# Performance work log

Hardware: AMD Instinct MI355X
Metric: run time of the kernel (lower is better)

The kernel has to match this reference:

```python
import jax, jax.numpy as jnp
import numpy as np

D_MODEL = 1024
NHEADS = 16
DK = D_MODEL // NHEADS  # 64
B, LQ, LK = 4, 1024, 1024


def setup_inputs() -> dict:
    key = jax.random.key(0)
    ks = jax.random.split(key, 5)
    q = jax.random.normal(ks[0], (B, LQ, NHEADS, DK), dtype=jnp.float32)
    k = jax.random.normal(ks[1], (B, LK, NHEADS, DK), dtype=jnp.float32)
    v = jax.random.normal(ks[2], (B, LK, NHEADS, DK), dtype=jnp.float32)
    # LazyLinear materializes with in_features = LK * NHEADS due to the
    # source bug (it projects the reshaped raw score tensor, not attn@V).
    fc_w = jax.random.normal(ks[3], (D_MODEL, LK * NHEADS), dtype=jnp.float32) * 0.02
    fc_b = jax.random.normal(ks[4], (D_MODEL,), dtype=jnp.float32) * 0.02
    return {"q": q, "k": k, "v": v, "fc_w": fc_w, "fc_b": fc_b}


def reference(q, k, v, fc_w, fc_b):
    # Raw scaled scores: [b, i, j, n]
    scores = jnp.einsum('bink,bjnk->bijn', q, k) / np.float32(np.sqrt(DK))
    # NOTE (faithful to source): the softmax(dim=1) and the attn@V einsum are
    # computed in the original but their result is discarded; the output is
    # built from the raw scores. v does not influence the output.
    b, i = scores.shape[0], scores.shape[1]
    out = scores.reshape(b, i, -1)            # [b, i, j*n]
    out = out @ fc_w.T + fc_b                 # Linear(j*n -> d_model)
    return out
```

## Files before the change

### kernel.cpp

```cpp
#include <hip/hip_runtime.h>
#include <hip/hip_bf16.h>


typedef unsigned short u16;
typedef unsigned int u32;
typedef __bf16 bf16x8 __attribute__((ext_vector_type(8)));
typedef float f32x4 __attribute__((ext_vector_type(4)));

__device__ __forceinline__ u16 f2bf(float f) {
  union { float f; unsigned u; } in;
  in.f = f;
  unsigned u = in.u;
  u += 0x7fffu + ((u >> 16) & 1u);
  return (u16)(u >> 16);
}

__global__ __launch_bounds__(256) void prep_qk(const float* __restrict__ q,
                                               const float* __restrict__ k,
                                               u16* __restrict__ Qb,
                                               u16* __restrict__ Kt) {
  __shared__ u16 lds[64][65];
  const int tid = threadIdx.x;
  const int bid = blockIdx.x;

  if (bid < 1024) {
    int idx = bid * 256 + tid;
    float4 r[4];
#pragma unroll
    for (int it = 0; it < 4; ++it)
      r[it] = reinterpret_cast<const float4*>(q)[it * 262144 + idx];
#pragma unroll
    for (int it = 0; it < 4; ++it) {
      ushort4 o;
      o.x = f2bf(r[it].x); o.y = f2bf(r[it].y);
      o.z = f2bf(r[it].z); o.w = f2bf(r[it].w);
      reinterpret_cast<ushort4*>(Qb)[it * 262144 + idx] = o;
    }
  } else {
    int e = bid - 1024;
    int jt = e & 15, n = (e >> 4) & 15, b = e >> 8;
    const int j0 = jt * 64;
    float4 r[4];
#pragma unroll
    for (int it = 0; it < 4; ++it) {
      int idx = it * 256 + tid;
      int jj = idx >> 4;
      int c4 = idx & 15;
      r[it] = *reinterpret_cast<const float4*>(
          &k[(((size_t)b * 1024 + j0 + jj) * 16 + n) * 64 + c4 * 4]);
    }
#pragma unroll
    for (int it = 0; it < 4; ++it) {
      int idx = it * 256 + tid;
      int jj = idx >> 4;
      int c4 = idx & 15;
      lds[c4 * 4 + 0][jj] = f2bf(r[it].x);
      lds[c4 * 4 + 1][jj] = f2bf(r[it].y);
      lds[c4 * 4 + 2][jj] = f2bf(r[it].z);
      lds[c4 * 4 + 3][jj] = f2bf(r[it].w);
    }
    __syncthreads();
    ushort4 o[4];
#pragma unroll
    for (int it = 0; it < 4; ++it) {
      int idx = it * 256 + tid;
      int kk = idx >> 4;
      int c4 = idx & 15;
      o[it].x = lds[kk][c4 * 4 + 0]; o[it].y = lds[kk][c4 * 4 + 1];
      o[it].z = lds[kk][c4 * 4 + 2]; o[it].w = lds[kk][c4 * 4 + 3];
    }
#pragma unroll
    for (int it = 0; it < 4; ++it) {
      int idx = it * 256 + tid;
      int kk = idx >> 4;
      int c4 = idx & 15;
      *reinterpret_cast<ushort4*>(
          &Kt[((size_t)n * 256 + b * 64 + kk) * 1024 + j0 + c4 * 4]) = o[it];
    }
  }
}

__global__ __launch_bounds__(256) void prep_w(const float* __restrict__ w,
                                              u16* __restrict__ Wt) {
  __shared__ u16 lds[16 * 520];
  u32* lds32 = reinterpret_cast<u32*>(lds);
  const int tid = threadIdx.x;
  const int d = blockIdx.x >> 1;
  const int h = blockIdx.x & 1;
  const float* src = w + (size_t)d * 16384 + h * 8192;

  float4 ra[4], rb[4];
  const int gbase = ((tid >> 2) << 3) + (tid & 3);
#pragma unroll
  for (int it = 0; it < 4; ++it) {
    int g1 = it * 512 + gbase;
    ra[it] = reinterpret_cast<const float4*>(src)[g1];
    rb[it] = reinterpret_cast<const float4*>(src)[g1 + 4];
  }
  const int n0 = (tid & 3) * 4;
#pragma unroll
  for (int it = 0; it < 4; ++it) {
    int a = (it * 512 + gbase) >> 2;
#pragma unroll
    for (int e = 0; e < 4; ++e) {
      float lo = (&ra[it].x)[e], hi = (&rb[it].x)[e];
      lds32[(n0 + e) * 260 + (a >> 1)] = (u32)f2bf(lo) | ((u32)f2bf(hi) << 16);
    }
  }
  __syncthreads();
  const int wv = tid >> 6, lane = tid & 63;
  ushort4 o[8];
#pragma unroll
  for (int s = 0; s < 8; ++s) {
    int row = 4 * wv + (s >> 1);
    int col = (s & 1) * 256 + lane * 4;
    o[s] = *reinterpret_cast<const ushort4*>(&lds[row * 520 + col]);
  }
#pragma unroll
  for (int s = 0; s < 8; ++s) {
    int row = 4 * wv + (s >> 1);
    int col = (s & 1) * 256 + lane * 4;
    *reinterpret_cast<ushort4*>(
        &Wt[(size_t)row * 1048576 + (size_t)d * 1024 + h * 512 + col]) = o[s];
  }
}

template <int VM>
__device__ __forceinline__ void waitVm() {
  if constexpr (VM == 16) asm volatile("s_waitcnt vmcnt(16)" ::: "memory");
  else if constexpr (VM == 8) asm volatile("s_waitcnt vmcnt(8)" ::: "memory");
  else asm volatile("s_waitcnt vmcnt(0)" ::: "memory");
}

template <int TN_TILES, int STAGE>
__global__ __launch_bounds__(256, 1) void gemm_bt(const u16* __restrict__ Abase,
                                                  const u16* __restrict__ Bbase,
                                                  u16* __restrict__ CoutBf,
                                                  float* __restrict__ CoutF,
                                                  const float* __restrict__ bias) {
  __shared__ u16 AB[4][2][128 * 64];
  const int tid = threadIdx.x;
  const int wid = tid >> 6;
  const int lane = tid & 63;
  const int batch = blockIdx.y;
  const int tm = blockIdx.x / TN_TILES;
  const int tn = blockIdx.x % TN_TILES;

  const u16* A = Abase + (size_t)batch * 1048576;
  const u16* B = Bbase + (size_t)batch * ((STAGE == 1) ? 262144 : 1048576);
  const int row0A = tm * 128, row0B = tn * 128;

  const int wr = wid >> 1;
  const int wc = wid & 1;
  const int laneRow = lane & 15;
  const int hi8 = (lane >> 4) * 8;
  const int swz = (lane & 7) * 8;

  f32x4 acc[4][4] = {};

  auto stage = [&](int tIdx) {
    const int kt = tIdx * 64;
    u16* lA = &AB[tIdx & 3][0][0];
    u16* lB = &AB[tIdx & 3][1][0];
#pragma unroll
    for (int i = 0; i < 4; ++i) {
      int p = i * 256 + tid;
      int r = p >> 3;
      int sc = ((p & 7) ^ (r & 7)) * 8;
      const u16* gA = A + (size_t)(row0A + r) * 1024 + kt + sc;
      const u16* gB = B + (size_t)(row0B + r) * 1024 + kt + sc;
      __builtin_amdgcn_global_load_lds(
          (const __attribute__((address_space(1))) void*)gA,
          (__attribute__((address_space(3))) void*)(lA + i * 2048 + wid * 512), 16, 0, 0);
      __builtin_amdgcn_global_load_lds(
          (const __attribute__((address_space(1))) void*)gB,
          (__attribute__((address_space(3))) void*)(lB + i * 2048 + wid * 512), 16, 0, 0);
    }
  };

  auto compute = [&](int tIdx) {
    const u16* At = &AB[tIdx & 3][0][0];
    const u16* Bt = &AB[tIdx & 3][1][0];
    bf16x8 af[2][4], bq[2][4];
#pragma unroll
    for (int kh = 0; kh < 2; ++kh) {
      int cs = (kh * 32 + hi8) ^ swz;
#pragma unroll
      for (int mi = 0; mi < 4; ++mi)
        af[kh][mi] = *reinterpret_cast<const bf16x8*>(
            &At[(wr * 64 + mi * 16 + laneRow) * 64 + cs]);
#pragma unroll
      for (int ni = 0; ni < 4; ++ni)
        bq[kh][ni] = *reinterpret_cast<const bf16x8*>(
            &Bt[(wc * 64 + ni * 16 + laneRow) * 64 + cs]);
    }
#pragma unroll
    for (int kh = 0; kh < 2; ++kh)
#pragma unroll
      for (int mi = 0; mi < 4; ++mi)
#pragma unroll
        for (int ni = 0; ni < 4; ++ni)
          acc[mi][ni] = __builtin_amdgcn_mfma_f32_16x16x32_bf16(
              af[kh][mi], bq[kh][ni], acc[mi][ni], 0, 0, 0);
  };

  stage(0); stage(1); stage(2);

  for (int t = 0; t < 13; ++t) {
    waitVm<16>();
    __builtin_amdgcn_s_barrier();
    stage(t + 3);
    compute(t);
  }
  waitVm<16>(); __builtin_amdgcn_s_barrier(); compute(13);
  waitVm<8>();  __builtin_amdgcn_s_barrier(); compute(14);
  waitVm<0>();  __builtin_amdgcn_s_barrier(); compute(15);

#pragma unroll
  for (int mi = 0; mi < 4; ++mi) {
#pragma unroll
    for (int ni = 0; ni < 4; ++ni) {
      int colg = tn * 128 + wc * 64 + ni * 16 + laneRow;
#pragma unroll
      for (int qq = 0; qq < 4; ++qq) {
        int rowg = tm * 128 + wr * 64 + mi * 16 + (lane >> 4) * 4 + qq;
        if (STAGE == 1) {
          size_t off = (size_t)(colg >> 6) * 1048576 + (size_t)rowg * 1024 +
                       (size_t)batch * 64 + (colg & 63);
          CoutBf[off] = f2bf(acc[mi][ni][qq]);
        } else {
          CoutF[(size_t)batch * 1048576 + (size_t)rowg * 1024 + colg] =
              acc[mi][ni][qq] * 0.125f + bias[colg];
        }
      }
    }
  }
}

extern "C" void kernel_launch(void* const* d_in, const int* in_sizes, int n_in,
                              void* d_out, int out_size, void* d_ws, size_t ws_size,
                              hipStream_t stream) {
  const float* q    = (const float*)d_in[0];
  const float* k    = (const float*)d_in[1];
  const float* fc_w = (const float*)d_in[3];
  const float* fc_b = (const float*)d_in[4];
  float* out = (float*)d_out;

  char* ws = (char*)d_ws;
  if (ws_size < 58720256) return;
  u16* Qb  = (u16*)(ws);
  u16* Kt  = (u16*)(ws + 8388608);
  u16* Wt  = (u16*)(ws + 16777216);
  u16* T2t = (u16*)(ws + 50331648);

  prep_qk<<<2048, 256, 0, stream>>>(q, k, Qb, Kt);
  prep_w<<<2048, 256, 0, stream>>>(fc_w, Wt);
  gemm_bt<2, 1><<<dim3(16, 16), 256, 0, stream>>>(Wt, Kt, T2t, nullptr, nullptr);
  gemm_bt<8, 2><<<dim3(64, 4), 256, 0, stream>>>(Qb, T2t, nullptr, out, fc_b);
}
```

Measured before the change: 64.04 us.

## Merge K and W prep kernels, move Q conversion into stage-1 GEMM tail

The K transpose and W transpose prep kernels are merged into a single launch, and the W store path now uses 16-byte vector stores instead of 8-byte ones. The Q fp32-to-bf16 conversion is moved out of the prep kernel and appended to the end of the first GEMM, with each of its 256 blocks converting a 64 KB slice. This removes one kernel launch and overlaps Q conversion with GEMM work. In exchange, the stage-1 GEMM blocks gain extra memory traffic at their tail.

```diff
diff --git a/kernel.cpp b/kernel.cpp
--- a/kernel.cpp
+++ b/kernel.cpp
@@ -6,6 +6,7 @@
 typedef unsigned int u32;
 typedef __bf16 bf16x8 __attribute__((ext_vector_type(8)));
 typedef float f32x4 __attribute__((ext_vector_type(4)));
+typedef u16 u16x8 __attribute__((ext_vector_type(8)));
 
 __device__ __forceinline__ u16 f2bf(float f) {
   union { float f; unsigned u; } in;
@@ -15,113 +16,92 @@
   return (u16)(u >> 16);
 }
 
-__global__ __launch_bounds__(256) void prep_qk(const float* __restrict__ q,
-                                               const float* __restrict__ k,
-                                               u16* __restrict__ Qb,
-                                               u16* __restrict__ Kt) {
-  __shared__ u16 lds[64][65];
+__global__ __launch_bounds__(256) void prep(const float* __restrict__ k,
+                                            const float* __restrict__ w,
+                                            u16* __restrict__ Kt,
+                                            u16* __restrict__ Wt) {
+  __shared__ u16 lds[16 * 520];
   const int tid = threadIdx.x;
   const int bid = blockIdx.x;
 
   if (bid < 1024) {
-    int idx = bid * 256 + tid;
+    int jt = bid & 15, n = (bid >> 4) & 15, b = bid >> 8;
+    auto l2 = reinterpret_cast<u16(*)[65]>(lds);
+    const int j0 = jt * 64;
     float4 r[4];
 #pragma unroll
-    for (int it = 0; it < 4; ++it)
-      r[it] = reinterpret_cast<const float4*>(q)[it * 262144 + idx];
-#pragma unroll
-    for (int it = 0; it < 4; ++it) {
-      ushort4 o;
-      o.x = f2bf(r[it].x); o.y = f2bf(r[it].y);
-      o.z = f2bf(r[it].z); o.w = f2bf(r[it].w);
-      reinterpret_cast<ushort4*>(Qb)[it * 262144 + idx] = o;
+    for (int it = 0; it < 4; ++it) {
+      int idx = it * 256 + tid;
+      int jj = idx >> 4;
+      int c4 = idx & 15;
+      r[it] = *reinterpret_cast<const float4*>(
+          &k[(((size_t)b * 1024 + j0 + jj) * 16 + n) * 64 + c4 * 4]);
+    }
+#pragma unroll
+    for (int it = 0; it < 4; ++it) {
+      int idx = it * 256 + tid;
+      int jj = idx >> 4;
+      int c4 = idx & 15;
+      l2[c4 * 4 + 0][jj] = f2bf(r[it].x);
+      l2[c4 * 4 + 1][jj] = f2bf(r[it].y);
+      l2[c4 * 4 + 2][jj] = f2bf(r[it].z);
+      l2[c4 * 4 + 3][jj] = f2bf(r[it].w);
+    }
+    __syncthreads();
+    ushort4 o[4];
+#pragma unroll
+    for (int it = 0; it < 4; ++it) {
+      int idx = it * 256 + tid;
+      int kk = idx >> 4;
+      int c4 = idx & 15;
+      o[it].x = l2[kk][c4 * 4 + 0]; o[it].y = l2[kk][c4 * 4 + 1];
+      o[it].z = l2[kk][c4 * 4 + 2]; o[it].w = l2[kk][c4 * 4 + 3];
+    }
+#pragma unroll
+    for (int it = 0; it < 4; ++it) {
+      int idx = it * 256 + tid;
+      int kk = idx >> 4;
+      int c4 = idx & 15;
+      *reinterpret_cast<ushort4*>(
+          &Kt[((size_t)n * 256 + b * 64 + kk) * 1024 + j0 + c4 * 4]) = o[it];
     }
   } else {
     int e = bid - 1024;
-    int jt = e & 15, n = (e >> 4) & 15, b = e >> 8;
-    const int j0 = jt * 64;
-    float4 r[4];
-#pragma unroll
-    for (int it = 0; it < 4; ++it) {
-      int idx = it * 256 + tid;
-      int jj = idx >> 4;
-      int c4 = idx & 15;
-      r[it] = *reinterpret_cast<const float4*>(
-          &k[(((size_t)b * 1024 + j0 + jj) * 16 + n) * 64 + c4 * 4]);
-    }
-#pragma unroll
-    for (int it = 0; it < 4; ++it) {
-      int idx = it * 256 + tid;
-      int jj = idx >> 4;
-      int c4 = idx & 15;
-      lds[c4 * 4 + 0][jj] = f2bf(r[it].x);
-      lds[c4 * 4 + 1][jj] = f2bf(r[it].y);
-      lds[c4 * 4 + 2][jj] = f2bf(r[it].z);
-      lds[c4 * 4 + 3][jj] = f2bf(r[it].w);
+    const int d = e >> 1;
+    const int h = e & 1;
+    u32* lds32 = reinterpret_cast<u32*>(lds);
+    const float* src = w + (size_t)d * 16384 + h * 8192;
+
+    float4 ra[4], rb[4];
+    const int gbase = ((tid >> 2) << 3) + (tid & 3);
+#pragma unroll
+    for (int it = 0; it < 4; ++it) {
+      int g1 = it * 512 + gbase;
+      ra[it] = reinterpret_cast<const float4*>(src)[g1];
+      rb[it] = reinterpret_cast<const float4*>(src)[g1 + 4];
+    }
+    const int n0 = (tid & 3) * 4;
+#pragma unroll
+    for (int it = 0; it < 4; ++it) {
+      int a = (it * 512 + gbase) >> 2;
+#pragma unroll
+      for (int el = 0; el < 4; ++el) {
+        float lo = (&ra[it].x)[el], hi = (&rb[it].x)[el];
+        lds32[(n0 + el) * 260 + (a >> 1)] = (u32)f2bf(lo) | ((u32)f2bf(hi) << 16);
+      }
     }
     __syncthreads();
-    ushort4 o[4];
-#pragma unroll
-    for (int it = 0; it < 4; ++it) {
-      int idx = it * 256 + tid;
-      int kk = idx >> 4;
-      int c4 = idx & 15;
-      o[it].x = lds[kk][c4 * 4 + 0]; o[it].y = lds[kk][c4 * 4 + 1];
-      o[it].z = lds[kk][c4 * 4 + 2]; o[it].w = lds[kk][c4 * 4 + 3];
-    }
-#pragma unroll
-    for (int it = 0; it < 4; ++it) {
-      int idx = it * 256 + tid;
-      int kk = idx >> 4;
-      int c4 = idx & 15;
-      *reinterpret_cast<ushort4*>(
-          &Kt[((size_t)n * 256 + b * 64 + kk) * 1024 + j0 + c4 * 4]) = o[it];
-    }
-  }
-}
-
-__global__ __launch_bounds__(256) void prep_w(const float* __restrict__ w,
-                                              u16* __restrict__ Wt) {
-  __shared__ u16 lds[16 * 520];
-  u32* lds32 = reinterpret_cast<u32*>(lds);
-  const int tid = threadIdx.x;
-  const int d = blockIdx.x >> 1;
-  const int h = blockIdx.x & 1;
-  const float* src = w + (size_t)d * 16384 + h * 8192;
-
-  float4 ra[4], rb[4];
-  const int gbase = ((tid >> 2) << 3) + (tid & 3);
-#pragma unroll
-  for (int it = 0; it < 4; ++it) {
-    int g1 = it * 512 + gbase;
-    ra[it] = reinterpret_cast<const float4*>(src)[g1];
-    rb[it] = reinterpret_cast<const float4*>(src)[g1 + 4];
-  }
-  const int n0 = (tid & 3) * 4;
-#pragma unroll
-  for (int it = 0; it < 4; ++it) {
-    int a = (it * 512 + gbase) >> 2;
-#pragma unroll
-    for (int e = 0; e < 4; ++e) {
-      float lo = (&ra[it].x)[e], hi = (&rb[it].x)[e];
-      lds32[(n0 + e) * 260 + (a >> 1)] = (u32)f2bf(lo) | ((u32)f2bf(hi) << 16);
-    }
-  }
-  __syncthreads();
-  const int wv = tid >> 6, lane = tid & 63;
-  ushort4 o[8];
-#pragma unroll
-  for (int s = 0; s < 8; ++s) {
-    int row = 4 * wv + (s >> 1);
-    int col = (s & 1) * 256 + lane * 4;
-    o[s] = *reinterpret_cast<const ushort4*>(&lds[row * 520 + col]);
-  }
-#pragma unroll
-  for (int s = 0; s < 8; ++s) {
-    int row = 4 * wv + (s >> 1);
-    int col = (s & 1) * 256 + lane * 4;
-    *reinterpret_cast<ushort4*>(
-        &Wt[(size_t)row * 1048576 + (size_t)d * 1024 + h * 512 + col]) = o[s];
+    const int wv = tid >> 6, lane = tid & 63;
+    u16x8 o[4];
+#pragma unroll
+    for (int s = 0; s < 4; ++s)
+      o[s] = *reinterpret_cast<const u16x8*>(&lds[(4 * wv + s) * 520 + lane * 8]);
+#pragma unroll
+    for (int s = 0; s < 4; ++s) {
+      int n = 4 * wv + s;
+      *reinterpret_cast<u16x8*>(
+          &Wt[(size_t)n * 1048576 + (size_t)d * 1024 + h * 512 + lane * 8]) = o[s];
+    }
   }
 }
 
@@ -137,7 +117,9 @@
                                                   const u16* __restrict__ Bbase,
                                                   u16* __restrict__ CoutBf,
                                                   float* __restrict__ CoutF,
-                                                  const float* __restrict__ bias) {
+                                                  const float* __restrict__ bias,
+                                                  const float* __restrict__ qsrc,
+                                                  u16* __restrict__ qdst) {
   __shared__ u16 AB[4][2][128 * 64];
   const int tid = threadIdx.x;
   const int wid = tid >> 6;
@@ -235,6 +217,25 @@
       }
     }
   }
+
+  if (STAGE == 1) {
+    const int cb = batch * 16 + blockIdx.x;
+    const float4* src = reinterpret_cast<const float4*>(qsrc) + (size_t)cb * 4096;
+    ushort4* dst = reinterpret_cast<ushort4*>(qdst) + (size_t)cb * 4096;
+#pragma unroll
+    for (int rnd = 0; rnd < 4; ++rnd) {
+      float4 r[4];
+#pragma unroll
+      for (int i = 0; i < 4; ++i) r[i] = src[rnd * 1024 + i * 256 + tid];
+#pragma unroll
+      for (int i = 0; i < 4; ++i) {
+        ushort4 o;
+        o.x = f2bf(r[i].x); o.y = f2bf(r[i].y);
+        o.z = f2bf(r[i].z); o.w = f2bf(r[i].w);
+        dst[rnd * 1024 + i * 256 + tid] = o;
+      }
+    }
+  }
 }
 
 extern "C" void kernel_launch(void* const* d_in, const int* in_sizes, int n_in,
@@ -253,8 +254,7 @@
   u16* Wt  = (u16*)(ws + 16777216);
   u16* T2t = (u16*)(ws + 50331648);
 
-  prep_qk<<<2048, 256, 0, stream>>>(q, k, Qb, Kt);
-  prep_w<<<2048, 256, 0, stream>>>(fc_w, Wt);
-  gemm_bt<2, 1><<<dim3(16, 16), 256, 0, stream>>>(Wt, Kt, T2t, nullptr, nullptr);
-  gemm_bt<8, 2><<<dim3(64, 4), 256, 0, stream>>>(Qb, T2t, nullptr, out, fc_b);
-}
+  prep<<<3072, 256, 0, stream>>>(k, fc_w, Kt, Wt);
+  gemm_bt<2, 1><<<dim3(16, 16), 256, 0, stream>>>(Wt, Kt, T2t, nullptr, nullptr, q, Qb);
+  gemm_bt<8, 2><<<dim3(64, 4), 256, 0, stream>>>(Qb, T2t, nullptr, out, fc_b, nullptr, nullptr);
+}
```

Result: faster. 60.57 us (-5.4%).
